# Kernel tuning notes

Hardware: AMD Instinct MI355X
Metric: run time of the kernel (lower is better)

Reference implementation:

```python
import jax, jax.numpy as jnp
import numpy as np

E = 64  # hidden size (hardcoded in the module)
D = 50  # embedding dim (hardcoded)


def lstm_scan(xs, h0, c0, Wih, Whh, b):
    """xs: (S, B, in). PyTorch gate order i, f, g, o."""
    def step(carry, x):
        h, c = carry
        g = x @ Wih.T + h @ Whh.T + b
        i, f, gg, o = jnp.split(g, 4, axis=-1)
        c = jax.nn.sigmoid(f) * c + jax.nn.sigmoid(i) * jnp.tanh(gg)
        h = jax.nn.sigmoid(o) * jnp.tanh(c)
        return (h, c), (h, c)
    _, (hs, cs) = jax.lax.scan(step, (h0, c0), xs)
    return hs, cs  # (S, B, E)


def setup_inputs() -> dict:
    key = jax.random.key(0)
    ks = iter(jax.random.split(key, 40))
    B, S, V = 64, 384, 100004
    f32 = jnp.float32

    def rn(shape, scale):
        return (jax.random.normal(next(ks), shape, dtype=f32) * scale)

    km = float(np.sqrt(2.0 / E))       # kaiming_normal fan_in=64
    lu = float(1.0 / np.sqrt(E))       # torch LSTM default init scale

    inp = {
        "sentence1": jax.random.randint(next(ks), (B, S), 0, V),
        "sentence2": jax.random.randint(next(ks), (B, S), 0, V),
        "s1_len": jax.random.randint(next(ks), (B, 1, E), 0, S),
        "s2_len": jax.random.randint(next(ks), (B, 1, E), 0, S),
        "s1_s": jnp.ones((B, S), dtype=f32),
        "s2_s": jnp.ones((B, S), dtype=f32),
        "emb": rn((V, D), 0.1),
        "Wih1": rn((4 * E, D), lu), "Whh1": rn((4 * E, E), lu),
        "bih1": rn((4 * E,), lu), "bhh1": rn((4 * E,), lu),
        "Wih2": rn((4 * E, D), lu), "Whh2": rn((4 * E, E), lu),
        "bih2": rn((4 * E,), lu), "bhh2": rn((4 * E,), lu),
        "wy": rn((E, E), km), "wh": rn((E, E), km),
        "w": rn((E,), 1.0),
        "wp": rn((E, E), km), "wx": rn((E, E), km),
        "wr": rn((E, E), km), "wt": rn((E, E), km),
        "l1_W": rn((128, E), km), "l1_b": jnp.zeros((128,), f32),
        "l_W": rn((4, 128), float(np.sqrt(2.0 / 128))), "l_b": jnp.zeros((4,), f32),
    }
    return inp


def reference(sentence1, sentence2, s1_len, s2_len, s1_s, s2_s, emb,
              Wih1, Whh1, bih1, bhh1, Wih2, Whh2, bih2, bhh2,
              wy, wh, w, wp, wx, wr, wt, l1_W, l1_b, l_W, l_b):
    B, S = sentence1.shape
    e1 = emb[sentence1]  # (B,S,50)
    e2 = emb[sentence2]
    h0 = jnp.zeros((B, E), e1.dtype)

    # LSTMCell loop over sentence1, collecting all h/c
    hs, cs = lstm_scan(e1.transpose(1, 0, 2), h0, h0, Wih1, Whh1, bih1 + bhh1)
    h = hs.transpose(1, 0, 2)  # (B,S,E)
    c = cs.transpose(1, 0, 2)

    # gather initial state for lstm2 at s1_len indices
    gh = jnp.take_along_axis(h, s1_len, axis=1)[:, 0, :]
    gc = jnp.take_along_axis(c, s1_len, axis=1)[:, 0, :]

    os_, _ = lstm_scan(e2.transpose(1, 0, 2), gh, gc, Wih2, Whh2, bih2 + bhh2)
    out = os_.transpose(1, 0, 2)  # (B,S,E); note s2 == s per expand semantics

    # wyy + whhn are loop-invariant in the original (out.expand is identity)
    base = jnp.einsum('bse,ef->bsf', h, wy) + jnp.einsum('bse,ef->bsf', out, wh)
    NEG = jnp.float32(1e12)

    def att_step(r, _):
        M = jnp.tanh(base + (r @ wr)[:, None, :])          # (B,S,E)
        score = jnp.einsum('bse,e->bs', M, w)              # (B,S)
        masked = s1_s * score - (1.0 - s1_s) * NEG
        soft = jax.nn.softmax(masked, axis=1)
        r_new = jnp.einsum('bse,bs->be', h, soft) + jnp.tanh(r @ wt)
        return r_new, r_new

    r0 = jnp.zeros((B, E), h.dtype)
    _, Rt = jax.lax.scan(att_step, r0, None, length=S)
    Rt = Rt.transpose(1, 0, 2)  # (B,S,E)

    rn_ = jnp.take_along_axis(Rt, s2_len, axis=1)[:, 0, :]
    hn = jnp.take_along_axis(out, s2_len, axis=1)[:, 0, :]
    hid = jnp.tanh(rn_ @ wp + hn @ wx)
    hid = jnp.tanh(hid @ l1_W.T + l1_b)   # Dropout is inference-mode identity
    return hid @ l_W.T + l_b              # (B,4)
```

## Files before the change

### kernel.cpp

```cpp
#include <hip/hip_runtime.h>

#define E 64
#define D 50
#define SS 384
#define G4 256

__device__ __forceinline__ float fast_rcp(float x){ return __builtin_amdgcn_rcpf(x); }
__device__ __forceinline__ float tanh_fast(float x){
  float e = __expf(2.0f*x);
  return 1.0f - 2.0f*fast_rcp(e + 1.0f);
}
__device__ __forceinline__ float sigmoid_fast(float x){
  return fast_rcp(1.0f + __expf(-x));
}
__device__ __forceinline__ float ror1(float x){
  return __int_as_float(__builtin_amdgcn_update_dpp(
      0, __float_as_int(x), 0x13C , 0xF, 0xF, false));
}
__device__ __forceinline__ float rdlane(float v, int l){
  return __int_as_float(__builtin_amdgcn_readlane(__float_as_int(v), l));
}
#define DPP0(x, ctrl) __int_as_float(__builtin_amdgcn_update_dpp( \
    0, __float_as_int(x), ctrl, 0xF, 0xF, true))
__device__ __forceinline__ float wave_sum64_l63(float x){
  x += DPP0(x, 0x111);
  x += DPP0(x, 0x112);
  x += DPP0(x, 0x114);
  x += DPP0(x, 0x118);
  x += DPP0(x, 0x142);
  x += DPP0(x, 0x143);
  return x;
}

__global__ __launch_bounds__(256, 1) void gx_kernel(
  const int* __restrict__ sent1, const int* __restrict__ sent2,
  const float* __restrict__ emb,
  const float* __restrict__ Wih1, const float* __restrict__ bih1, const float* __restrict__ bhh1,
  const float* __restrict__ Wih2, const float* __restrict__ bih2, const float* __restrict__ bhh2,
  float* __restrict__ gx1, float* __restrict__ gx2)
{
  const int bb    = blockIdx.x;
  const int which = bb >> 8;
  const int chunk = bb & 255;
  const int j     = threadIdx.x;
  const int*   sent = which ? sent2 : sent1;
  const float* Wih  = which ? Wih2  : Wih1;
  const float* bA   = which ? bih2  : bih1;
  const float* bB   = which ? bhh2  : bhh1;
  float*       gx   = which ? gx2   : gx1;

  float wih[D];
  #pragma unroll
  for (int k=0;k<D;k+=2){
    float2 v = *(const float2*)&Wih[j*D+k];
    wih[k]=v.x; wih[k+1]=v.y;
  }
  const float bias = bA[j] + bB[j];

  __shared__ __align__(16) float xb[8][52];
  const int row0 = chunk*96;
  for (int c=0;c<12;++c){
    const int r0 = row0 + c*8;
    #pragma unroll
    for (int q=0;q<2;++q){
      int tt = j + q*256;
      if (tt < 400){
        int r = tt/50;
        int k = tt - r*50;
        int idx = sent[r0 + r];
        xb[r][k] = emb[(size_t)idx*D + k];
      }
    }
    __syncthreads();
    for (int r=0;r<8;++r){
      float a0=bias, a1=0.f;
      #pragma unroll
      for (int k=0;k<48;k+=4){
        float4 xv = *(const float4*)&xb[r][k];
        a0 += xv.x*wih[k]   + xv.y*wih[k+1];
        a1 += xv.z*wih[k+2] + xv.w*wih[k+3];
      }
      a0 += xb[r][48]*wih[48];
      a1 += xb[r][49]*wih[49];
      gx[(size_t)(r0+r)*G4 + j] = a0+a1;
    }
    __syncthreads();
  }
}

__global__ __launch_bounds__(256, 1) void lstm_kernel(
  const float* __restrict__ gx1, const float* __restrict__ gx2,
  const float* __restrict__ Whh1, const float* __restrict__ Whh2,
  const int* __restrict__ s1_len, const int* __restrict__ s2_len,
  float* __restrict__ h1_all, float* __restrict__ out_all,
  float* __restrict__ hn_cap)
{
  const int b = blockIdx.x;
  const int j = threadIdx.x;
  const int lane = j & 63;
  const int wv = j >> 6;
  __shared__ float gates[2][256];

  float whht[64];
  #pragma unroll
  for (int i=0;i<32;++i){
    whht[i]    = Whh1[j*64 + ((lane-i)&63)];
    whht[i+32] = Whh1[j*64 + ((lane-i+32)&63)];
  }

  const int is_g = (wv==2);
  float c_reg=0.f, h_reg=0.f, gh=0.f, gc=0.f, hn=0.f;
  const int idx1 = s1_len[b*64+lane];
  const int idx2 = s2_len[b*64+lane];

  {
    const float* gx = gx1 + (size_t)b*SS*G4;
    float* hout = h1_all + (size_t)b*SS*E;
    float gx_cur = gx[j];
    float gx_n1  = gx[G4 + j];
    for (int s=0;s<SS;++s){
      int sn2 = (s+2<SS)? s+2 : SS-1;
      float gx_n2 = gx[(size_t)sn2*G4 + j];
      float hr  = h_reg;
      float hr2 = __shfl_xor(h_reg, 32);
      float g0 = gx_cur, g1 = 0.f;
      #pragma unroll
      for (int i=0;i<32;++i){
        g0 = __builtin_fmaf(hr,  whht[i],    g0);
        g1 = __builtin_fmaf(hr2, whht[i+32], g1);
        hr = ror1(hr); hr2 = ror1(hr2);
      }
      float g = g0 + g1;
      const int p = s & 1;
      gates[p][j] = is_g ? tanh_fast(g) : sigmoid_fast(g);
      __syncthreads();
      float gi=gates[p][lane], gf=gates[p][64+lane], gg=gates[p][128+lane], go=gates[p][192+lane];
      c_reg = gf*c_reg + gi*gg;
      h_reg = go * tanh_fast(c_reg);
      if (wv==0) hout[(size_t)s*E + lane] = h_reg;
      if (s==idx1){ gh=h_reg; gc=c_reg; }
      gx_cur = gx_n1; gx_n1 = gx_n2;
    }
  }
  #pragma unroll
  for (int i=0;i<32;++i){
    whht[i]    = Whh2[j*64 + ((lane-i)&63)];
    whht[i+32] = Whh2[j*64 + ((lane-i+32)&63)];
  }
  h_reg = gh; c_reg = gc;
  __syncthreads();
  {
    const float* gx = gx2 + (size_t)b*SS*G4;
    float* hout = out_all + (size_t)b*SS*E;
    float gx_cur = gx[j];
    float gx_n1  = gx[G4 + j];
    for (int s=0;s<SS;++s){
      int sn2 = (s+2<SS)? s+2 : SS-1;
      float gx_n2 = gx[(size_t)sn2*G4 + j];
      float hr  = h_reg;
      float hr2 = __shfl_xor(h_reg, 32);
      float g0 = gx_cur, g1 = 0.f;
      #pragma unroll
      for (int i=0;i<32;++i){
        g0 = __builtin_fmaf(hr,  whht[i],    g0);
        g1 = __builtin_fmaf(hr2, whht[i+32], g1);
        hr = ror1(hr); hr2 = ror1(hr2);
      }
      float g = g0 + g1;
      const int p = s & 1;
      gates[p][j] = is_g ? tanh_fast(g) : sigmoid_fast(g);
      __syncthreads();
      float gi=gates[p][lane], gf=gates[p][64+lane], gg=gates[p][128+lane], go=gates[p][192+lane];
      c_reg = gf*c_reg + gi*gg;
      h_reg = go * tanh_fast(c_reg);
      if (wv==0) hout[(size_t)s*E + lane] = h_reg;
      if (s==idx2) hn = h_reg;
      gx_cur = gx_n1; gx_n1 = gx_n2;
    }
  }
  if (wv==0) hn_cap[b*64+lane] = hn;
}

__global__ __launch_bounds__(256, 1) void base_kernel(
  const float* __restrict__ h1_all, const float* __restrict__ out_all,
  const float* __restrict__ wy, const float* __restrict__ wh,
  float* __restrict__ E_g)
{
  const int t = threadIdx.x;
  const int wave = t>>6, lane = t&63;
  float wyc[E], whc[E];
  #pragma unroll
  for (int e=0;e<E;++e){ wyc[e]=wy[e*E+lane]; whc[e]=wh[e*E+lane]; }
  const int row0 = blockIdx.x*16 + wave*4;
  for (int r=0;r<4;++r){
    int row = row0 + r;
    float hv = h1_all[(size_t)row*E + lane];
    float ov = out_all[(size_t)row*E + lane];
    float a0=0,a1=0;
    #pragma unroll
    for (int e=0;e<E;++e){
      a0 += rdlane(hv,e)*wyc[e];
      a1 += rdlane(ov,e)*whc[e];
    }
    E_g[(size_t)row*E + lane] = __expf(2.0f*(a0+a1));
  }
}

__global__ __launch_bounds__(384, 1) void attn_kernel(
  const float* __restrict__ h1_all, const float* __restrict__ E_all,
  const float* __restrict__ w, const float* __restrict__ wr, const float* __restrict__ wt,
  const float* __restrict__ s1_s, const int* __restrict__ s2_len,
  float* __restrict__ rn_cap)
{
  const int b = blockIdx.x;
  const int t = threadIdx.x;
  const int wv = t>>6, lane = t&63;
  const int row = wv*64 + lane;

  __shared__ float  accP[6*64];
  __shared__ float  totP[8];
  __shared__ float2 rwrtP[6*64];

  const float* h1b = h1_all + (size_t)b*SS*E;
  const float* Eb  = E_all  + (size_t)b*SS*E;

  float Ee[64];
  #pragma unroll
  for (int k=0;k<64;k+=4){
    float4 v = *(const float4*)&Eb[(size_t)row*E + k];
    Ee[k]=v.x; Ee[k+1]=v.y; Ee[k+2]=v.z; Ee[k+3]=v.w;
  }
  float ht[64];
  #pragma unroll
  for (int i=0;i<32;++i){
    ht[i]    = h1b[(size_t)(wv*64 + ((lane-i)&63))*E + lane];
    ht[i+32] = h1b[(size_t)(wv*64 + ((lane-i+32)&63))*E + lane];
  }
  float WSUM = 0.f;
  for (int e=0;e<64;++e) WSUM += w[e];
  const float s1v = s1_s[b*SS + row];
  const int  idx2 = s2_len[b*E + lane];
  const int k0  = (wv<4)? wv*11 : 44+(wv-4)*10;
  const int cnt = (wv<4)? 11 : 10;
  float wrch[11], wtch[11];
  #pragma unroll
  for (int jj=0;jj<11;++jj){
    int kk = k0 + ((jj<cnt)? jj : 0);
    wrch[jj] = wr[kk*E + lane];
    wtch[jj] = wt[kk*E + lane];
  }

  rwrtP[t] = make_float2(0.f, 0.f);
  __syncthreads();

  float rn_keep = 0.f;
  for (int s=0;s<SS;++s){
    float rwl=0.f, rtl=0.f;
    #pragma unroll
    for (int q=0;q<6;++q){ float2 v = rwrtP[q*64+lane]; rwl+=v.x; rtl+=v.y; }
    float Rl = __expf(2.0f*rwl);

    float sc0=0.f, sc1=0.f;
    #pragma unroll
    for (int e=0;e<64;e+=4){
      float r0=rdlane(Rl,e),   r1=rdlane(Rl,e+1);
      float r2=rdlane(Rl,e+2), r3=rdlane(Rl,e+3);
      float A  = __builtin_fmaf(Ee[e],  r0, 1.f);
      float B  = __builtin_fmaf(Ee[e+1],r1, 1.f);
      float C  = __builtin_fmaf(Ee[e+2],r2, 1.f);
      float Dv = __builtin_fmaf(Ee[e+3],r3, 1.f);
      float n0 = __builtin_fmaf(w[e],   B,  w[e+1]*A);
      float n1 = __builtin_fmaf(w[e+2], Dv, w[e+3]*C);
      sc0 = __builtin_fmaf(n0, fast_rcp(A*B),  sc0);
      sc1 = __builtin_fmaf(n1, fast_rcp(C*Dv), sc1);
    }
    float sc = WSUM - 2.0f*(sc0+sc1);
    float masked = s1v*sc - (1.f - s1v)*1e12f;
    float ex = __expf(masked);

    float exr  = ex;
    float exr2 = __shfl_xor(ex, 32);
    float acc=0.f;
    #pragma unroll
    for (int i=0;i<32;++i){
      acc = __builtin_fmaf(exr,  ht[i],    acc);
      acc = __builtin_fmaf(exr2, ht[i+32], acc);
      exr = ror1(exr); exr2 = ror1(exr2);
    }
    accP[wv*64+lane] = acc;
    float tw = wave_sum64_l63(ex);
    if (lane==63) totP[wv] = tw;
    __syncthreads();

    float av=0.f;
    #pragma unroll
    for (int q=0;q<6;++q) av += accP[q*64+lane];
    float tv = ((totP[0]+totP[1])+(totP[2]+totP[3]))+(totP[4]+totP[5]);
    float rnew = __builtin_fmaf(av, fast_rcp(tv), tanh_fast(rtl));
    if (wv==0 && s==idx2) rn_keep = rnew;
    float rwp=0.f, rtp=0.f;
    #pragma unroll
    for (int jj=0;jj<11;++jj){
      if (jj<cnt){
        float rv = rdlane(rnew, k0+jj);
        rwp = __builtin_fmaf(rv, wrch[jj], rwp);
        rtp = __builtin_fmaf(rv, wtch[jj], rtp);
      }
    }
    rwrtP[wv*64+lane] = make_float2(rwp, rtp);
    __syncthreads();
  }
  if (wv==0) rn_cap[b*E + lane] = rn_keep;
}

__global__ __launch_bounds__(128, 1) void final_kernel(
  const float* __restrict__ rn_cap, const float* __restrict__ hn_cap,
  const float* __restrict__ wp, const float* __restrict__ wx,
  const float* __restrict__ l1W, const float* __restrict__ l1b,
  const float* __restrict__ lW, const float* __restrict__ lb,
  float* __restrict__ out)
{
  const int b = blockIdx.x, t = threadIdx.x;
  __shared__ float rn[E], hn[E], hid1[E], hid2[128];
  if (t<E){ rn[t]=rn_cap[b*E+t]; hn[t]=hn_cap[b*E+t]; }
  __syncthreads();
  if (t<E){
    float a0=0,a1=0;
    #pragma unroll
    for (int k=0;k<E;++k){
      a0 += rn[k]*wp[k*E+t];
      a1 += hn[k]*wx[k*E+t];
    }
    hid1[t] = tanh_fast(a0+a1);
  }
  __syncthreads();
  {
    float acc = l1b[t];
    #pragma unroll
    for (int k=0;k<E;++k) acc += hid1[k]*l1W[t*E+k];
    hid2[t] = tanh_fast(acc);
  }
  __syncthreads();
  if (t<4){
    float acc = lb[t];
    #pragma unroll
    for (int k=0;k<128;++k) acc += hid2[k]*lW[t*128+k];
    out[b*4+t] = acc;
  }
}

extern "C" void kernel_launch(void* const* d_in, const int* in_sizes, int n_in,
                              void* d_out, int out_size, void* d_ws, size_t ws_size,
                              hipStream_t stream)
{
  const int*   sent1 = (const int*)  d_in[0];
  const int*   sent2 = (const int*)  d_in[1];
  const int*   s1len = (const int*)  d_in[2];
  const int*   s2len = (const int*)  d_in[3];
  const float* s1s   = (const float*)d_in[4];
  const float* emb   = (const float*)d_in[6];
  const float* Wih1  = (const float*)d_in[7];
  const float* Whh1  = (const float*)d_in[8];
  const float* bih1  = (const float*)d_in[9];
  const float* bhh1  = (const float*)d_in[10];
  const float* Wih2  = (const float*)d_in[11];
  const float* Whh2  = (const float*)d_in[12];
  const float* bih2  = (const float*)d_in[13];
  const float* bhh2  = (const float*)d_in[14];
  const float* wy    = (const float*)d_in[15];
  const float* wh    = (const float*)d_in[16];
  const float* w     = (const float*)d_in[17];
  const float* wp    = (const float*)d_in[18];
  const float* wx    = (const float*)d_in[19];
  const float* wr    = (const float*)d_in[20];
  const float* wt    = (const float*)d_in[21];
  const float* l1W   = (const float*)d_in[22];
  const float* l1b   = (const float*)d_in[23];
  const float* lW    = (const float*)d_in[24];
  const float* lb    = (const float*)d_in[25];
  float* out = (float*)d_out;

  float* ws  = (float*)d_ws;
  float* gx1 = ws;
  float* gx2 = gx1 + 6291456;
  float* h1  = gx2 + 6291456;
  float* outa= h1  + 1572864;
  float* Eg  = outa + 1572864;
  float* rnc = Eg  + 1572864;
  float* hnc = rnc + 4096;

  hipLaunchKernelGGL(gx_kernel, dim3(512), dim3(256), 0, stream,
    sent1, sent2, emb, Wih1, bih1, bhh1, Wih2, bih2, bhh2, gx1, gx2);
  hipLaunchKernelGGL(lstm_kernel, dim3(64), dim3(256), 0, stream,
    gx1, gx2, Whh1, Whh2, s1len, s2len, h1, outa, hnc);
  hipLaunchKernelGGL(base_kernel, dim3(1536), dim3(256), 0, stream,
    h1, outa, wy, wh, Eg);
  hipLaunchKernelGGL(attn_kernel, dim3(64), dim3(384), 0, stream,
    h1, Eg, w, wr, wt, s1s, s2len, rnc);
  hipLaunchKernelGGL(final_kernel, dim3(64), dim3(128), 0, stream,
    rnc, hnc, wp, wx, l1W, l1b, lW, lb, out);
}
```

Before: 1.652 ms.

## Replace DPP rotate broadcasts with LDS float4 broadcasts in LSTM and attention

The LSTM recurrence, the attention score loop and the weighted-sum loop now broadcast per-lane values through wave-private shared-memory buffers read as float4, instead of DPP row-rotate chains and readlane. Weights are stored in natural order, and four independent FMA accumulators replace two. The aim is to shorten the serial dependency chain of DPP moves on each timestep. In exchange it adds LDS writes and reads each step. Correctness relies on each wave reading only its own buffer, so no extra barrier is needed.

Result: faster. 1.327 ms (-19.7%).

```diff
diff --git a/kernel.cpp b/kernel.cpp
--- a/kernel.cpp
+++ b/kernel.cpp
@@ -12,10 +12,6 @@
 }
 __device__ __forceinline__ float sigmoid_fast(float x){
   return fast_rcp(1.0f + __expf(-x));
-}
-__device__ __forceinline__ float ror1(float x){
-  return __int_as_float(__builtin_amdgcn_update_dpp(
-      0, __float_as_int(x), 0x13C , 0xF, 0xF, false));
 }
 __device__ __forceinline__ float rdlane(float v, int l){
   return __int_as_float(__builtin_amdgcn_readlane(__float_as_int(v), l));
@@ -100,18 +96,20 @@
   const int lane = j & 63;
   const int wv = j >> 6;
   __shared__ float gates[2][256];
-
-  float whht[64];
-  #pragma unroll
-  for (int i=0;i<32;++i){
-    whht[i]    = Whh1[j*64 + ((lane-i)&63)];
-    whht[i+32] = Whh1[j*64 + ((lane-i+32)&63)];
+  __shared__ __align__(16) float hbuf[4][64];
+
+  float whr[64];
+  #pragma unroll
+  for (int k=0;k<64;k+=4){
+    float4 v = *(const float4*)&Whh1[j*64+k];
+    whr[k]=v.x; whr[k+1]=v.y; whr[k+2]=v.z; whr[k+3]=v.w;
   }
 
   const int is_g = (wv==2);
   float c_reg=0.f, h_reg=0.f, gh=0.f, gc=0.f, hn=0.f;
   const int idx1 = s1_len[b*64+lane];
   const int idx2 = s2_len[b*64+lane];
+  hbuf[wv][lane] = 0.f;
 
   {
     const float* gx = gx1 + (size_t)b*SS*G4;
@@ -121,33 +119,35 @@
     for (int s=0;s<SS;++s){
       int sn2 = (s+2<SS)? s+2 : SS-1;
       float gx_n2 = gx[(size_t)sn2*G4 + j];
-      float hr  = h_reg;
-      float hr2 = __shfl_xor(h_reg, 32);
-      float g0 = gx_cur, g1 = 0.f;
+      float g0=gx_cur, g1=0.f, g2=0.f, g3=0.f;
       #pragma unroll
-      for (int i=0;i<32;++i){
-        g0 = __builtin_fmaf(hr,  whht[i],    g0);
-        g1 = __builtin_fmaf(hr2, whht[i+32], g1);
-        hr = ror1(hr); hr2 = ror1(hr2);
+      for (int k=0;k<64;k+=4){
+        float4 hv = *(const float4*)&hbuf[wv][k];
+        g0 = __builtin_fmaf(hv.x, whr[k],   g0);
+        g1 = __builtin_fmaf(hv.y, whr[k+1], g1);
+        g2 = __builtin_fmaf(hv.z, whr[k+2], g2);
+        g3 = __builtin_fmaf(hv.w, whr[k+3], g3);
       }
-      float g = g0 + g1;
+      float g = (g0+g1)+(g2+g3);
       const int p = s & 1;
       gates[p][j] = is_g ? tanh_fast(g) : sigmoid_fast(g);
       __syncthreads();
       float gi=gates[p][lane], gf=gates[p][64+lane], gg=gates[p][128+lane], go=gates[p][192+lane];
       c_reg = gf*c_reg + gi*gg;
       h_reg = go * tanh_fast(c_reg);
+      hbuf[wv][lane] = h_reg;
       if (wv==0) hout[(size_t)s*E + lane] = h_reg;
       if (s==idx1){ gh=h_reg; gc=c_reg; }
       gx_cur = gx_n1; gx_n1 = gx_n2;
     }
   }
   #pragma unroll
-  for (int i=0;i<32;++i){
-    whht[i]    = Whh2[j*64 + ((lane-i)&63)];
-    whht[i+32] = Whh2[j*64 + ((lane-i+32)&63)];
+  for (int k=0;k<64;k+=4){
+    float4 v = *(const float4*)&Whh2[j*64+k];
+    whr[k]=v.x; whr[k+1]=v.y; whr[k+2]=v.z; whr[k+3]=v.w;
   }
   h_reg = gh; c_reg = gc;
+  hbuf[wv][lane] = gh;
   __syncthreads();
   {
     const float* gx = gx2 + (size_t)b*SS*G4;
@@ -157,22 +157,23 @@
     for (int s=0;s<SS;++s){
       int sn2 = (s+2<SS)? s+2 : SS-1;
       float gx_n2 = gx[(size_t)sn2*G4 + j];
-      float hr  = h_reg;
-      float hr2 = __shfl_xor(h_reg, 32);
-      float g0 = gx_cur, g1 = 0.f;
+      float g0=gx_cur, g1=0.f, g2=0.f, g3=0.f;
       #pragma unroll
-      for (int i=0;i<32;++i){
-        g0 = __builtin_fmaf(hr,  whht[i],    g0);
-        g1 = __builtin_fmaf(hr2, whht[i+32], g1);
-        hr = ror1(hr); hr2 = ror1(hr2);
+      for (int k=0;k<64;k+=4){
+        float4 hv = *(const float4*)&hbuf[wv][k];
+        g0 = __builtin_fmaf(hv.x, whr[k],   g0);
+        g1 = __builtin_fmaf(hv.y, whr[k+1], g1);
+        g2 = __builtin_fmaf(hv.z, whr[k+2], g2);
+        g3 = __builtin_fmaf(hv.w, whr[k+3], g3);
       }
-      float g = g0 + g1;
+      float g = (g0+g1)+(g2+g3);
       const int p = s & 1;
       gates[p][j] = is_g ? tanh_fast(g) : sigmoid_fast(g);
       __syncthreads();
       float gi=gates[p][lane], gf=gates[p][64+lane], gg=gates[p][128+lane], go=gates[p][192+lane];
       c_reg = gf*c_reg + gi*gg;
       h_reg = go * tanh_fast(c_reg);
+      hbuf[wv][lane] = h_reg;
       if (wv==0) hout[(size_t)s*E + lane] = h_reg;
       if (s==idx2) hn = h_reg;
       gx_cur = gx_n1; gx_n1 = gx_n2;
@@ -220,6 +221,8 @@
   __shared__ float  accP[6*64];
   __shared__ float  totP[8];
   __shared__ float2 rwrtP[6*64];
+  __shared__ __align__(16) float exL[6][64];
+  __shared__ __align__(16) float RlL[6][64];
 
   const float* h1b = h1_all + (size_t)b*SS*E;
   const float* Eb  = E_all  + (size_t)b*SS*E;
@@ -232,9 +235,8 @@
   }
   float ht[64];
   #pragma unroll
-  for (int i=0;i<32;++i){
-    ht[i]    = h1b[(size_t)(wv*64 + ((lane-i)&63))*E + lane];
-    ht[i+32] = h1b[(size_t)(wv*64 + ((lane-i+32)&63))*E + lane];
+  for (int i=0;i<64;++i){
+    ht[i] = h1b[(size_t)(wv*64 + i)*E + lane];
   }
   float WSUM = 0.f;
   for (int e=0;e<64;++e) WSUM += w[e];
@@ -259,35 +261,45 @@
     #pragma unroll
     for (int q=0;q<6;++q){ float2 v = rwrtP[q*64+lane]; rwl+=v.x; rtl+=v.y; }
     float Rl = __expf(2.0f*rwl);
-
-    float sc0=0.f, sc1=0.f;
-    #pragma unroll
-    for (int e=0;e<64;e+=4){
-      float r0=rdlane(Rl,e),   r1=rdlane(Rl,e+1);
-      float r2=rdlane(Rl,e+2), r3=rdlane(Rl,e+3);
-      float A  = __builtin_fmaf(Ee[e],  r0, 1.f);
-      float B  = __builtin_fmaf(Ee[e+1],r1, 1.f);
-      float C  = __builtin_fmaf(Ee[e+2],r2, 1.f);
-      float Dv = __builtin_fmaf(Ee[e+3],r3, 1.f);
+    RlL[wv][lane] = Rl;
+
+    float sc0=0.f, sc1=0.f, sc2=0.f, sc3=0.f;
+    #pragma unroll
+    for (int e=0;e<64;e+=8){
+      float4 ra = *(const float4*)&RlL[wv][e];
+      float4 rb = *(const float4*)&RlL[wv][e+4];
+      float A  = __builtin_fmaf(Ee[e],  ra.x, 1.f);
+      float B  = __builtin_fmaf(Ee[e+1],ra.y, 1.f);
+      float C  = __builtin_fmaf(Ee[e+2],ra.z, 1.f);
+      float Dv = __builtin_fmaf(Ee[e+3],ra.w, 1.f);
       float n0 = __builtin_fmaf(w[e],   B,  w[e+1]*A);
       float n1 = __builtin_fmaf(w[e+2], Dv, w[e+3]*C);
       sc0 = __builtin_fmaf(n0, fast_rcp(A*B),  sc0);
       sc1 = __builtin_fmaf(n1, fast_rcp(C*Dv), sc1);
-    }
-    float sc = WSUM - 2.0f*(sc0+sc1);
+      float A2  = __builtin_fmaf(Ee[e+4], rb.x, 1.f);
+      float B2  = __builtin_fmaf(Ee[e+5], rb.y, 1.f);
+      float C2  = __builtin_fmaf(Ee[e+6], rb.z, 1.f);
+      float D2  = __builtin_fmaf(Ee[e+7], rb.w, 1.f);
+      float n2 = __builtin_fmaf(w[e+4], B2, w[e+5]*A2);
+      float n3 = __builtin_fmaf(w[e+6], D2, w[e+7]*C2);
+      sc2 = __builtin_fmaf(n2, fast_rcp(A2*B2), sc2);
+      sc3 = __builtin_fmaf(n3, fast_rcp(C2*D2), sc3);
+    }
+    float sc = WSUM - 2.0f*((sc0+sc1)+(sc2+sc3));
     float masked = s1v*sc - (1.f - s1v)*1e12f;
     float ex = __expf(masked);
 
-    float exr  = ex;
-    float exr2 = __shfl_xor(ex, 32);
-    float acc=0.f;
-    #pragma unroll
-    for (int i=0;i<32;++i){
-      acc = __builtin_fmaf(exr,  ht[i],    acc);
-      acc = __builtin_fmaf(exr2, ht[i+32], acc);
-      exr = ror1(exr); exr2 = ror1(exr2);
-    }
-    accP[wv*64+lane] = acc;
+    exL[wv][lane] = ex;
+    float a0=0.f, a1=0.f, a2=0.f, a3=0.f;
+    #pragma unroll
+    for (int i=0;i<64;i+=4){
+      float4 v = *(const float4*)&exL[wv][i];
+      a0 = __builtin_fmaf(v.x, ht[i],   a0);
+      a1 = __builtin_fmaf(v.y, ht[i+1], a1);
+      a2 = __builtin_fmaf(v.z, ht[i+2], a2);
+      a3 = __builtin_fmaf(v.w, ht[i+3], a3);
+    }
+    accP[wv*64+lane] = (a0+a1)+(a2+a3);
     float tw = wave_sum64_l63(ex);
     if (lane==63) totP[wv] = tw;
     __syncthreads();
```
